# Kernel optimization log

Hardware: AMD Instinct MI355X
Metric: run time of the kernel (lower is better)

Reference implementation:

```python
import jax, jax.numpy as jnp
import numpy as np

B, T, TOKEN_DIM, TPR_DIM = 16, 256, 256, 10
INNER = TOKEN_DIM // 4  # 64
TH = 32                 # tpr_mlp hidden dim
EPS = 1e-5              # BatchNorm eps


def _bn(x, g, b, m, v):
    # BatchNorm1d in eval mode: normalize with running stats
    return (x - m) * jax.lax.rsqrt(v + EPS) * g + b


def setup_inputs() -> dict:
    key = jax.random.key(0)
    ks = iter(jax.random.split(key, 32))
    def n(shape, s=0.02):
        return jax.random.normal(next(ks), shape, dtype=jnp.float32) * s
    def bn_params(c):
        g = 1.0 + 0.1 * jax.random.normal(next(ks), (c,), dtype=jnp.float32)
        b = 0.1 * jax.random.normal(next(ks), (c,), dtype=jnp.float32)
        m = 0.1 * jax.random.normal(next(ks), (c,), dtype=jnp.float32)
        v = jax.random.uniform(next(ks), (c,), dtype=jnp.float32, minval=0.5, maxval=1.5)
        return g, b, m, v
    inp = {}
    inp['x'] = jax.random.normal(next(ks), (B, T, TOKEN_DIM), dtype=jnp.float32)
    inp['r'] = jax.random.normal(next(ks), (B, T, T, TPR_DIM), dtype=jnp.float32)
    # fc1: Linear(token,token) + BN(token)
    inp['W1'] = n((TOKEN_DIM, TOKEN_DIM)); inp['b1'] = n((TOKEN_DIM,))
    inp['bn1_g'], inp['bn1_b'], inp['bn1_m'], inp['bn1_v'] = bn_params(TOKEN_DIM)
    # VectorAttention
    inp['Wqkv'] = n((TOKEN_DIM, 3 * INNER))
    inp['Wt1'] = n((TPR_DIM, TH)); inp['bt1'] = n((TH,))
    inp['bnt_g'], inp['bnt_b'], inp['bnt_m'], inp['bnt_v'] = bn_params(TH)
    inp['Wt2'] = n((TH, INNER)); inp['bt2'] = n((INNER,))
    inp['Wa1'] = n((INNER, INNER)); inp['ba1'] = n((INNER,))
    inp['Wa2'] = n((INNER, INNER)); inp['ba2'] = n((INNER,))
    # fc2: Linear(inner, token) + BN(token)
    inp['W2'] = n((INNER, TOKEN_DIM)); inp['b2'] = n((TOKEN_DIM,))
    inp['bn2_g'], inp['bn2_b'], inp['bn2_m'], inp['bn2_v'] = bn_params(TOKEN_DIM)
    return inp


def reference(x, r, W1, b1, bn1_g, bn1_b, bn1_m, bn1_v, Wqkv,
              Wt1, bt1, bnt_g, bnt_b, bnt_m, bnt_v, Wt2, bt2,
              Wa1, ba1, Wa2, ba2, W2, b2, bn2_g, bn2_b, bn2_m, bn2_v):
    # fc1 + BN, residual skip (pre-relu)
    y = _bn(x @ W1 + b1, bn1_g, bn1_b, bn1_m, bn1_v)  # [B,T,C]
    skip = y
    y = jax.nn.relu(y)
    # VectorAttention
    qkv = y @ Wqkv                                     # [B,T,3*inner]
    q, k, v = jnp.split(qkv, 3, axis=-1)               # each [B,T,inner]
    qk_rel = q[:, :, None, :] - k[:, None, :, :]       # [B,T,T,inner]
    rel_emb = jax.nn.relu(_bn(r @ Wt1 + bt1, bnt_g, bnt_b, bnt_m, bnt_v)) @ Wt2 + bt2  # [B,T,T,inner]
    vv = v[:, None, :, :] + rel_emb                    # [B,T,T,inner]
    h = jax.nn.relu((qk_rel + rel_emb) @ Wa1 + ba1)
    sim = h @ Wa2 + ba2                                # [B,T,T,inner]
    attn = jax.nn.softmax(sim, axis=-2)                # softmax over j (neighbor) axis
    agg = jnp.sum(attn * vv, axis=2)                   # [B,T,inner]
    # fc2 + BN + residual + relu
    out = jax.nn.relu(_bn(agg @ W2 + b2, bn2_g, bn2_b, bn2_m, bn2_v) + skip)
    return out  # [B,T,token_dim]
```

## Files before the change

### kernel.cpp

```cpp
#include <hip/hip_runtime.h>
#include <hip/hip_bf16.h>
#include <math.h>

#define BB 16
#define TT 256
#define CC 256
#define INNER 64
#define TPR 10
#define THD 32
#define EPSV 1e-5f

typedef __attribute__((ext_vector_type(8))) short short8;
typedef __attribute__((ext_vector_type(4))) float f32x4;

__device__ __forceinline__ short f2bf(float f) {
    unsigned u = __float_as_uint(f);
    u += 0x7fffu + ((u >> 16) & 1);
    return (short)(u >> 16);
}
__device__ __forceinline__ unsigned cvtpk(float a, float b) {
    __hip_bfloat162 h = __float22bfloat162_rn(float2{a, b});
    return *(unsigned*)&h;
}

#define IMG_WT1  0
#define IMG_WT2  2048
#define IMG_WA1  6144
#define IMG_WA2  14336
#define IMG_C1   22528
#define IMG_SZ   22656

__device__ __forceinline__ int sww(int pb, int key) {
    return ((pb & ~15) ^ key) | (pb & 15);
}

__global__ __launch_bounds__(256) void prep_kernel(
    const float* __restrict__ Wt1, const float* __restrict__ bt1,
    const float* __restrict__ gt, const float* __restrict__ bbt,
    const float* __restrict__ mt, const float* __restrict__ vt,
    const float* __restrict__ Wt2, const float* __restrict__ Wa1,
    const float* __restrict__ Wa2, char* __restrict__ img)
{
    const int blk = blockIdx.x, t = threadIdx.x;
    if (blk == 0) {
        for (int e = t; e < 32 * 32; e += 256) {
            int m = e >> 5, k = e & 31;
            float scv = gt[m] * rsqrtf(vt[m] + EPSV);
            float v = (k < TPR) ? Wt1[k * 32 + m] * scv : 0.f;
            *(short*)(img + IMG_WT1 + m * 64 + k * 2) = f2bf(v);
        }
        if (t < 32) {
            float scv = gt[t] * rsqrtf(vt[t] + EPSV);
            ((float*)(img + IMG_C1))[t] = (bt1[t] - mt[t]) * scv + bbt[t];
        }
    } else if (blk == 1) {
        for (int e = t; e < 32 * 64; e += 256) {
            int h = e >> 6, c = e & 63;
            int off = IMG_WT2 + (c >> 1) * 128 + sww((c & 1) * 64 + h * 2, ((c >> 1) & 7) << 4);
            *(short*)(img + off) = f2bf(Wt2[e]);
        }
    } else {
        const float* W = (blk == 2) ? Wa1 : Wa2;
        int base = (blk == 2) ? IMG_WA1 : IMG_WA2;
        for (int e = t; e < 64 * 64; e += 256) {
            int k = e >> 6, c = e & 63;
            int off = base + c * 128 + sww(k * 2, (c & 7) << 4);
            *(short*)(img + off) = f2bf(W[e]);
        }
    }
}

__global__ __launch_bounds__(256) void fc1_qkv_kernel(
    const float* __restrict__ x, const float* __restrict__ W1, const float* __restrict__ b1,
    const float* __restrict__ g1, const float* __restrict__ bb1,
    const float* __restrict__ m1, const float* __restrict__ v1,
    const float* __restrict__ Wqkv,
    float* __restrict__ skip, float* __restrict__ qkv)
{
    const int ROWS = 8;
    __shared__ float xr[ROWS][CC];
    __shared__ float yr[ROWS][CC];
    const int n0 = blockIdx.x * ROWS;
    const int t = threadIdx.x;

#pragma unroll
    for (int rr = 0; rr < ROWS; ++rr)
        xr[rr][t] = x[(size_t)(n0 + rr) * CC + t];
    __syncthreads();

    float acc[ROWS];
#pragma unroll
    for (int rr = 0; rr < ROWS; ++rr) acc[rr] = 0.f;
    for (int k = 0; k < CC; ++k) {
        float wv = W1[(size_t)k * CC + t];
#pragma unroll
        for (int rr = 0; rr < ROWS; ++rr) acc[rr] = fmaf(xr[rr][k], wv, acc[rr]);
    }
    const float s1 = g1[t] * rsqrtf(v1[t] + EPSV);
    const float base = b1[t] - m1[t];
    const float bet = bb1[t];
#pragma unroll
    for (int rr = 0; rr < ROWS; ++rr) {
        float y = (acc[rr] + base) * s1 + bet;
        skip[(size_t)(n0 + rr) * CC + t] = y;
        yr[rr][t] = fmaxf(y, 0.f);
    }
    __syncthreads();

    if (t < 192) {
        float a2[ROWS];
#pragma unroll
        for (int rr = 0; rr < ROWS; ++rr) a2[rr] = 0.f;
        for (int k = 0; k < CC; ++k) {
            float wv = Wqkv[(size_t)k * 192 + t];
#pragma unroll
            for (int rr = 0; rr < ROWS; ++rr) a2[rr] = fmaf(yr[rr][k], wv, a2[rr]);
        }
#pragma unroll
        for (int rr = 0; rr < ROWS; ++rr)
            qkv[(size_t)(n0 + rr) * 192 + t] = a2[rr];
    }
}

#define O_R    0
#define O_TH   16384
#define O_WT1  49152
#define O_WT2  51200
#define O_WA1  55296
#define O_WA2  63488
#define O_RED  71680
#define LDSZ   75776

__device__ __forceinline__ int swb(int row, int cb, int sh, int mask) {
    return (row << sh) + (((cb & ~15) ^ ((row & mask) << 4)) | (cb & 15));
}
__device__ __forceinline__ short8 ldfrag(const char* lds, int base, int row, int cb16, int sh, int mask) {
    return *(const short8*)(lds + base + (row << sh) + (cb16 ^ ((row & mask) << 4)));
}

__global__ __launch_bounds__(512, 4) void attn_mfma_kernel(
    const float* __restrict__ r, const float* __restrict__ qkv,
    const float* __restrict__ bt2, const float* __restrict__ ba1,
    const char* __restrict__ img, float* __restrict__ agg)
{
    __shared__ __align__(16) char lds[LDSZ];
    const int n = blockIdx.x, b = n >> 8;
    const int tid = threadIdx.x;
    const int wv = tid >> 6, lane = tid & 63;
    const int lid = lane & 15, q4 = lane >> 4;
    const int kb = q4 * 16;
    const int jt0 = wv * 2;

    const float* kvb = qkv + (size_t)b * (TT * 192);
    const f32x4 z4 = {0.f, 0.f, 0.f, 0.f};

#pragma unroll
    for (int ci = 0; ci < 3; ++ci) {
        int c = wv + ci * 8;
        if (c < 22) {
            int ldsoff;
            if (c < 2)       ldsoff = O_WT1 + c * 1024;
            else if (c < 6)  ldsoff = O_WT2 + (c - 2) * 1024;
            else if (c < 14) ldsoff = O_WA1 + (c - 6) * 1024;
            else             ldsoff = O_WA2 + (c - 14) * 1024;
            __builtin_amdgcn_global_load_lds(
                (const __attribute__((address_space(1))) unsigned*)(const unsigned*)(img + c * 1024 + lane * 16),
                (__attribute__((address_space(3))) unsigned*)(unsigned*)(lds + ldsoff + lane * 16),
                16, 0, 0);
        }
    }

    f32x4 k4[4][2];
#pragma unroll
    for (int tm = 0; tm < 4; ++tm) {
        int ch0 = tm * 16 + q4 * 4;
#pragma unroll
        for (int tn = 0; tn < 2; ++tn) {
            int j = (jt0 + tn) * 16 + lid;
            k4[tm][tn] = *(const f32x4*)(kvb + (size_t)j * 192 + 64 + ch0);
        }
    }

    {
        const float* rrow = r + (size_t)n * (TT * TPR);
        int j = tid >> 1, half = tid & 1;
        const float* rp = rrow + j * TPR + half * 5;
        float v0 = rp[0], v1 = rp[1], v2 = rp[2], v3 = rp[3], v4 = rp[4];
        char* rb = lds + O_R + j * 64;
        if (half == 0) {
            uint2 w; w.x = cvtpk(v0, v1); w.y = cvtpk(v2, v3);
            *(uint2*)(rb) = w;
            *(unsigned short*)(rb + 8) = (unsigned short)f2bf(v4);
        } else {
            *(unsigned short*)(rb + 10) = (unsigned short)f2bf(v0);
            *(unsigned*)(rb + 12) = cvtpk(v1, v2);
            *(unsigned*)(rb + 16) = cvtpk(v3, v4);
            *(unsigned*)(rb + 20) = 0u;
            uint2 zz; zz.x = 0u; zz.y = 0u;
            *(uint2*)(rb + 24) = zz;
            *(uint2*)(rb + 32) = zz;
            *(uint2*)(rb + 40) = zz;
            *(uint2*)(rb + 48) = zz;
            *(uint2*)(rb + 56) = zz;
        }
    }
    __syncthreads();

    const float* c1g = (const float*)(img + IMG_C1);

    {
        short8 a10 = ldfrag(lds, O_WT1, lid, kb, 6, 0);
        short8 a11 = ldfrag(lds, O_WT1, 16 + lid, kb, 6, 0);
        f32x4 c1v0 = *(const f32x4*)(c1g + q4 * 4);
        f32x4 c1v1 = *(const f32x4*)(c1g + 16 + q4 * 4);
        f32x4 acc1[2][2];
#pragma unroll
        for (int tn = 0; tn < 2; ++tn) {
            int j = (jt0 + tn) * 16 + lid;
            short8 bf = ldfrag(lds, O_R, j, kb, 6, 0);
            acc1[0][tn] = __builtin_amdgcn_mfma_f32_16x16x32_bf16(a10, bf, c1v0, 0, 0, 0);
            acc1[1][tn] = __builtin_amdgcn_mfma_f32_16x16x32_bf16(a11, bf, c1v1, 0, 0, 0);
        }
#pragma unroll
        for (int tm = 0; tm < 2; ++tm)
#pragma unroll
            for (int tn = 0; tn < 2; ++tn) {
                int j = (jt0 + tn) * 16 + lid;
                uint2 w;
                w.x = cvtpk(fmaxf(acc1[tm][tn][0], 0.f), fmaxf(acc1[tm][tn][1], 0.f));
                w.y = cvtpk(fmaxf(acc1[tm][tn][2], 0.f), fmaxf(acc1[tm][tn][3], 0.f));
                *(uint2*)(lds + O_TH + swb(j, tm * 32 + q4 * 8, 7, 7)) = w;
            }
    }

    f32x4 qv4[4], bt2v[4];
#pragma unroll
    for (int tm = 0; tm < 4; ++tm) {
        int ch0 = tm * 16 + q4 * 4;
        qv4[tm] = *(const f32x4*)(qkv + (size_t)n * 192 + ch0);
        bt2v[tm] = *(const f32x4*)(bt2 + ch0);
    }

    f32x4 rel[4][2];
    {
        short8 aw[4];
#pragma unroll
        for (int tm = 0; tm < 4; ++tm) {
            int c = tm * 16 + lid;
            aw[tm] = ldfrag(lds, O_WT2, c >> 1, (c & 1) * 64 + kb, 7, 7);
        }
#pragma unroll
        for (int tn = 0; tn < 2; ++tn) {
            int j = (jt0 + tn) * 16 + lid;
            short8 bf = ldfrag(lds, O_TH, j, kb, 7, 7);
#pragma unroll
            for (int tm = 0; tm < 4; ++tm)
                rel[tm][tn] = __builtin_amdgcn_mfma_f32_16x16x32_bf16(aw[tm], bf, bt2v[tm], 0, 0, 0);
        }
    }
#pragma unroll
    for (int tm = 0; tm < 4; ++tm)
#pragma unroll
        for (int tn = 0; tn < 2; ++tn) {
            int j = (jt0 + tn) * 16 + lid;
            float t0 = qv4[tm][0] - k4[tm][tn][0] + rel[tm][tn][0];
            float t1 = qv4[tm][1] - k4[tm][tn][1] + rel[tm][tn][1];
            float t2 = qv4[tm][2] - k4[tm][tn][2] + rel[tm][tn][2];
            float t3 = qv4[tm][3] - k4[tm][tn][3] + rel[tm][tn][3];
            uint2 w; w.x = cvtpk(t0, t1); w.y = cvtpk(t2, t3);
            *(uint2*)(lds + O_TH + swb(j, tm * 32 + q4 * 8, 7, 7)) = w;
        }

    f32x4 ba1v[4];
#pragma unroll
    for (int tm = 0; tm < 4; ++tm)
        ba1v[tm] = *(const f32x4*)(ba1 + tm * 16 + q4 * 4);
    f32x4 acc[4][2];
#pragma unroll
    for (int tm = 0; tm < 4; ++tm)
#pragma unroll
        for (int tn = 0; tn < 2; ++tn) acc[tm][tn] = ba1v[tm];
#pragma unroll
    for (int ks = 0; ks < 2; ++ks) {
        short8 aw[4];
#pragma unroll
        for (int tm = 0; tm < 4; ++tm)
            aw[tm] = ldfrag(lds, O_WA1, tm * 16 + lid, ks * 64 + kb, 7, 7);
#pragma unroll
        for (int tn = 0; tn < 2; ++tn) {
            int j = (jt0 + tn) * 16 + lid;
            short8 bf = ldfrag(lds, O_TH, j, ks * 64 + kb, 7, 7);
#pragma unroll
            for (int tm = 0; tm < 4; ++tm)
                acc[tm][tn] = __builtin_amdgcn_mfma_f32_16x16x32_bf16(aw[tm], bf, acc[tm][tn], 0, 0, 0);
        }
    }

    f32x4 v4h[4][2];
#pragma unroll
    for (int tm = 0; tm < 4; ++tm) {
        int ch0 = tm * 16 + q4 * 4;
#pragma unroll
        for (int tn = 0; tn < 2; ++tn) {
            int j = (jt0 + tn) * 16 + lid;
            v4h[tm][tn] = *(const f32x4*)(kvb + (size_t)j * 192 + 128 + ch0);
        }
    }

#pragma unroll
    for (int tm = 0; tm < 4; ++tm)
#pragma unroll
        for (int tn = 0; tn < 2; ++tn) {
            int j = (jt0 + tn) * 16 + lid;
            uint2 w;
            w.x = cvtpk(fmaxf(acc[tm][tn][0], 0.f), fmaxf(acc[tm][tn][1], 0.f));
            w.y = cvtpk(fmaxf(acc[tm][tn][2], 0.f), fmaxf(acc[tm][tn][3], 0.f));
            *(uint2*)(lds + O_TH + swb(j, tm * 32 + q4 * 8, 7, 7)) = w;
        }

#pragma unroll
    for (int tm = 0; tm < 4; ++tm)
#pragma unroll
        for (int tn = 0; tn < 2; ++tn) acc[tm][tn] = z4;
#pragma unroll
    for (int ks = 0; ks < 2; ++ks) {
        short8 aw[4];
#pragma unroll
        for (int tm = 0; tm < 4; ++tm)
            aw[tm] = ldfrag(lds, O_WA2, tm * 16 + lid, ks * 64 + kb, 7, 7);
#pragma unroll
        for (int tn = 0; tn < 2; ++tn) {
            int j = (jt0 + tn) * 16 + lid;
            short8 bf = ldfrag(lds, O_TH, j, ks * 64 + kb, 7, 7);
#pragma unroll
            for (int tm = 0; tm < 4; ++tm)
                acc[tm][tn] = __builtin_amdgcn_mfma_f32_16x16x32_bf16(aw[tm], bf, acc[tm][tn], 0, 0, 0);
        }
    }

#pragma unroll
    for (int tm = 0; tm < 4; ++tm) {
        f32x4 num = z4, den = z4;
#pragma unroll
        for (int tn = 0; tn < 2; ++tn) {
#pragma unroll
            for (int g = 0; g < 4; ++g) {
                float ev = __expf(acc[tm][tn][g]);
                den[g] += ev;
                num[g] = fmaf(ev, v4h[tm][tn][g] + rel[tm][tn][g], num[g]);
            }
        }
#pragma unroll
        for (int ofs = 1; ofs < 16; ofs <<= 1) {
#pragma unroll
            for (int g = 0; g < 4; ++g) {
                num[g] += __shfl_xor(num[g], ofs);
                den[g] += __shfl_xor(den[g], ofs);
            }
        }
        if (lid == 0) {
            int base = O_RED + ((wv * 4 + tm) * 4 + q4) * 32;
            *(f32x4*)(lds + base) = num;
            *(f32x4*)(lds + base + 16) = den;
        }
    }
    __syncthreads();

    if (tid < 64) {
        int tm = tid >> 4, qq = (tid >> 2) & 3, g = tid & 3;
        float nn = 0.f, dd = 0.f;
#pragma unroll
        for (int w = 0; w < 8; ++w) {
            int base = O_RED + ((w * 4 + tm) * 4 + qq) * 32 + g * 4;
            nn += *(const float*)(lds + base);
            dd += *(const float*)(lds + base + 16);
        }
        agg[(size_t)n * 64 + tid] = nn / dd;
    }
}

__global__ __launch_bounds__(256) void fc2_kernel(
    const float* __restrict__ agg, const float* __restrict__ W2, const float* __restrict__ b2,
    const float* __restrict__ g2, const float* __restrict__ bb2,
    const float* __restrict__ m2, const float* __restrict__ v2,
    const float* __restrict__ skip, float* __restrict__ out)
{
    const int ROWS = 8;
    __shared__ float ar[ROWS][INNER];
    const int n0 = blockIdx.x * ROWS;
    const int t = threadIdx.x;

    for (int idx = t; idx < ROWS * INNER; idx += 256)
        ((float*)ar)[idx] = agg[(size_t)n0 * INNER + idx];
    __syncthreads();

    const float s2 = g2[t] * rsqrtf(v2[t] + EPSV);
    const float base = b2[t] - m2[t];
    const float bet = bb2[t];

    float accv[ROWS];
#pragma unroll
    for (int rr = 0; rr < ROWS; ++rr) accv[rr] = 0.f;
    for (int k = 0; k < INNER; ++k) {
        float wv = W2[(size_t)k * CC + t];
#pragma unroll
        for (int rr = 0; rr < ROWS; ++rr) accv[rr] = fmaf(ar[rr][k], wv, accv[rr]);
    }
#pragma unroll
    for (int rr = 0; rr < ROWS; ++rr) {
        float y = (accv[rr] + base) * s2 + bet;
        out[(size_t)(n0 + rr) * CC + t] =
            fmaxf(y + skip[(size_t)(n0 + rr) * CC + t], 0.f);
    }
}

extern "C" void kernel_launch(void* const* d_in, const int* in_sizes, int n_in,
                              void* d_out, int out_size, void* d_ws, size_t ws_size,
                              hipStream_t stream)
{
    const float* x   = (const float*)d_in[0];
    const float* r   = (const float*)d_in[1];
    const float* W1  = (const float*)d_in[2];
    const float* b1  = (const float*)d_in[3];
    const float* g1  = (const float*)d_in[4];
    const float* bb1 = (const float*)d_in[5];
    const float* m1  = (const float*)d_in[6];
    const float* v1  = (const float*)d_in[7];
    const float* Wqkv= (const float*)d_in[8];
    const float* Wt1 = (const float*)d_in[9];
    const float* bt1 = (const float*)d_in[10];
    const float* gt  = (const float*)d_in[11];
    const float* bbt = (const float*)d_in[12];
    const float* mt  = (const float*)d_in[13];
    const float* vt  = (const float*)d_in[14];
    const float* Wt2 = (const float*)d_in[15];
    const float* bt2 = (const float*)d_in[16];
    const float* Wa1 = (const float*)d_in[17];
    const float* ba1 = (const float*)d_in[18];
    const float* Wa2 = (const float*)d_in[19];
    const float* W2  = (const float*)d_in[21];
    const float* b2  = (const float*)d_in[22];
    const float* g2  = (const float*)d_in[23];
    const float* bb2 = (const float*)d_in[24];
    const float* m2  = (const float*)d_in[25];
    const float* v2  = (const float*)d_in[26];
    float* out = (float*)d_out;

    const int N = BB * TT;
    float* skip = (float*)d_ws;
    float* qkv  = skip + (size_t)N * CC;
    float* agg  = qkv  + (size_t)N * 192;
    char*  img  = (char*)(agg + (size_t)N * 64);

    prep_kernel<<<dim3(4), dim3(256), 0, stream>>>(
        Wt1, bt1, gt, bbt, mt, vt, Wt2, Wa1, Wa2, img);
    fc1_qkv_kernel<<<dim3(N / 8), dim3(256), 0, stream>>>(
        x, W1, b1, g1, bb1, m1, v1, Wqkv, skip, qkv);
    attn_mfma_kernel<<<dim3(N), dim3(512), 0, stream>>>(
        r, qkv, bt2, ba1, img, agg);
    fc2_kernel<<<dim3(N / 8), dim3(256), 0, stream>>>(
        agg, W2, b2, g2, bb2, m2, v2, skip, out);
}
```

Measured before the change: 160.5 us.

## Pack q-k and v+rel into bf16 registers, pad r rows, relax launch bounds

```diff
diff --git a/kernel.cpp b/kernel.cpp
--- a/kernel.cpp
+++ b/kernel.cpp
@@ -12,6 +12,7 @@
 
 typedef __attribute__((ext_vector_type(8))) short short8;
 typedef __attribute__((ext_vector_type(4))) float f32x4;
+typedef __attribute__((ext_vector_type(4))) unsigned int u32x4;
 
 __device__ __forceinline__ short f2bf(float f) {
     unsigned u = __float_as_uint(f);
@@ -22,6 +23,8 @@
     __hip_bfloat162 h = __float22bfloat162_rn(float2{a, b});
     return *(unsigned*)&h;
 }
+__device__ __forceinline__ float bf_lo(unsigned u) { return __uint_as_float(u << 16); }
+__device__ __forceinline__ float bf_hi(unsigned u) { return __uint_as_float(u & 0xffff0000u); }
 
 #define IMG_WT1  0
 #define IMG_WT2  2048
@@ -123,13 +126,13 @@
 }
 
 #define O_R    0
-#define O_TH   16384
-#define O_WT1  49152
-#define O_WT2  51200
-#define O_WA1  55296
-#define O_WA2  63488
-#define O_RED  71680
-#define LDSZ   75776
+#define O_TH   20480
+#define O_WT1  53248
+#define O_WT2  55296
+#define O_WA1  59392
+#define O_WA2  67584
+#define O_RED  75776
+#define LDSZ   79872
 
 __device__ __forceinline__ int swb(int row, int cb, int sh, int mask) {
     return (row << sh) + (((cb & ~15) ^ ((row & mask) << 4)) | (cb & 15));
@@ -138,7 +141,7 @@
     return *(const short8*)(lds + base + (row << sh) + (cb16 ^ ((row & mask) << 4)));
 }
 
-__global__ __launch_bounds__(512, 4) void attn_mfma_kernel(
+__global__ __launch_bounds__(512, 2) void attn_mfma_kernel(
     const float* __restrict__ r, const float* __restrict__ qkv,
     const float* __restrict__ bt2, const float* __restrict__ ba1,
     const char* __restrict__ img, float* __restrict__ agg)
@@ -170,10 +173,11 @@
         }
     }
 
-    f32x4 k4[4][2];
+    f32x4 qv4[4], k4[4][2];
 #pragma unroll
     for (int tm = 0; tm < 4; ++tm) {
         int ch0 = tm * 16 + q4 * 4;
+        qv4[tm] = *(const f32x4*)(qkv + (size_t)n * 192 + ch0);
 #pragma unroll
         for (int tn = 0; tn < 2; ++tn) {
             int j = (jt0 + tn) * 16 + lid;
@@ -183,25 +187,25 @@
 
     {
         const float* rrow = r + (size_t)n * (TT * TPR);
-        int j = tid >> 1, half = tid & 1;
-        const float* rp = rrow + j * TPR + half * 5;
+        int j = tid >> 1, hf = tid & 1;
+        const float* rp = rrow + j * TPR + hf * 5;
         float v0 = rp[0], v1 = rp[1], v2 = rp[2], v3 = rp[3], v4 = rp[4];
-        char* rb = lds + O_R + j * 64;
-        if (half == 0) {
-            uint2 w; w.x = cvtpk(v0, v1); w.y = cvtpk(v2, v3);
-            *(uint2*)(rb) = w;
-            *(unsigned short*)(rb + 8) = (unsigned short)f2bf(v4);
+        float o0 = __shfl_xor(v0, 1);
+        float o1 = __shfl_xor(v1, 1);
+        float o2 = __shfl_xor(v2, 1);
+        char* rb = lds + O_R + j * 80;
+        u32x4 z = {0u, 0u, 0u, 0u};
+        if (hf == 0) {
+            u32x4 c;
+            c[0] = cvtpk(v0, v1); c[1] = cvtpk(v2, v3);
+            c[2] = cvtpk(v4, o0); c[3] = cvtpk(o1, o2);
+            *(u32x4*)(rb) = c;
+            *(u32x4*)(rb + 32) = z;
         } else {
-            *(unsigned short*)(rb + 10) = (unsigned short)f2bf(v0);
-            *(unsigned*)(rb + 12) = cvtpk(v1, v2);
-            *(unsigned*)(rb + 16) = cvtpk(v3, v4);
-            *(unsigned*)(rb + 20) = 0u;
-            uint2 zz; zz.x = 0u; zz.y = 0u;
-            *(uint2*)(rb + 24) = zz;
-            *(uint2*)(rb + 32) = zz;
-            *(uint2*)(rb + 40) = zz;
-            *(uint2*)(rb + 48) = zz;
-            *(uint2*)(rb + 56) = zz;
+            u32x4 c;
+            c[0] = cvtpk(v3, v4); c[1] = 0u; c[2] = 0u; c[3] = 0u;
+            *(u32x4*)(rb + 16) = c;
+            *(u32x4*)(rb + 48) = z;
         }
     }
     __syncthreads();
@@ -209,15 +213,15 @@
     const float* c1g = (const float*)(img + IMG_C1);
 
     {
-        short8 a10 = ldfrag(lds, O_WT1, lid, kb, 6, 0);
-        short8 a11 = ldfrag(lds, O_WT1, 16 + lid, kb, 6, 0);
+        short8 a10 = *(const short8*)(lds + O_WT1 + lid * 64 + kb);
+        short8 a11 = *(const short8*)(lds + O_WT1 + (16 + lid) * 64 + kb);
         f32x4 c1v0 = *(const f32x4*)(c1g + q4 * 4);
         f32x4 c1v1 = *(const f32x4*)(c1g + 16 + q4 * 4);
         f32x4 acc1[2][2];
 #pragma unroll
         for (int tn = 0; tn < 2; ++tn) {
             int j = (jt0 + tn) * 16 + lid;
-            short8 bf = ldfrag(lds, O_R, j, kb, 6, 0);
+            short8 bf = *(const short8*)(lds + O_R + j * 80 + kb);
             acc1[0][tn] = __builtin_amdgcn_mfma_f32_16x16x32_bf16(a10, bf, c1v0, 0, 0, 0);
             acc1[1][tn] = __builtin_amdgcn_mfma_f32_16x16x32_bf16(a11, bf, c1v1, 0, 0, 0);
         }
@@ -233,12 +237,25 @@
             }
     }
 
-    f32x4 qv4[4], bt2v[4];
+    uint2 pk[4][2];
+#pragma unroll
+    for (int tm = 0; tm < 4; ++tm)
+#pragma unroll
+        for (int tn = 0; tn < 2; ++tn) {
+            pk[tm][tn].x = cvtpk(qv4[tm][0] - k4[tm][tn][0], qv4[tm][1] - k4[tm][tn][1]);
+            pk[tm][tn].y = cvtpk(qv4[tm][2] - k4[tm][tn][2], qv4[tm][3] - k4[tm][tn][3]);
+        }
+
+    f32x4 v4h[4][2], bt2v[4];
 #pragma unroll
     for (int tm = 0; tm < 4; ++tm) {
         int ch0 = tm * 16 + q4 * 4;
-        qv4[tm] = *(const f32x4*)(qkv + (size_t)n * 192 + ch0);
         bt2v[tm] = *(const f32x4*)(bt2 + ch0);
+#pragma unroll
+        for (int tn = 0; tn < 2; ++tn) {
+            int j = (jt0 + tn) * 16 + lid;
+            v4h[tm][tn] = *(const f32x4*)(kvb + (size_t)j * 192 + 128 + ch0);
+        }
     }
 
     f32x4 rel[4][2];
@@ -258,17 +275,23 @@
                 rel[tm][tn] = __builtin_amdgcn_mfma_f32_16x16x32_bf16(aw[tm], bf, bt2v[tm], 0, 0, 0);
         }
     }
-#pragma unroll
-    for (int tm = 0; tm < 4; ++tm)
-#pragma unroll
-        for (int tn = 0; tn < 2; ++tn) {
-            int j = (jt0 + tn) * 16 + lid;
-            float t0 = qv4[tm][0] - k4[tm][tn][0] + rel[tm][tn][0];
-            float t1 = qv4[tm][1] - k4[tm][tn][1] + rel[tm][tn][1];
-            float t2 = qv4[tm][2] - k4[tm][tn][2] + rel[tm][tn][2];
-            float t3 = qv4[tm][3] - k4[tm][tn][3] + rel[tm][tn][3];
+
+    uint2 vvp[4][2];
+#pragma unroll
+    for (int tm = 0; tm < 4; ++tm)
+#pragma unroll
+        for (int tn = 0; tn < 2; ++tn) {
+            int j = (jt0 + tn) * 16 + lid;
+            float r0 = rel[tm][tn][0], r1 = rel[tm][tn][1];
+            float r2 = rel[tm][tn][2], r3 = rel[tm][tn][3];
+            float t0 = bf_lo(pk[tm][tn].x) + r0;
+            float t1 = bf_hi(pk[tm][tn].x) + r1;
+            float t2 = bf_lo(pk[tm][tn].y) + r2;
+            float t3 = bf_hi(pk[tm][tn].y) + r3;
             uint2 w; w.x = cvtpk(t0, t1); w.y = cvtpk(t2, t3);
             *(uint2*)(lds + O_TH + swb(j, tm * 32 + q4 * 8, 7, 7)) = w;
+            vvp[tm][tn].x = cvtpk(v4h[tm][tn][0] + r0, v4h[tm][tn][1] + r1);
+            vvp[tm][tn].y = cvtpk(v4h[tm][tn][2] + r2, v4h[tm][tn][3] + r3);
         }
 
     f32x4 ba1v[4];
@@ -295,18 +318,6 @@
                 acc[tm][tn] = __builtin_amdgcn_mfma_f32_16x16x32_bf16(aw[tm], bf, acc[tm][tn], 0, 0, 0);
         }
     }
-
-    f32x4 v4h[4][2];
-#pragma unroll
-    for (int tm = 0; tm < 4; ++tm) {
-        int ch0 = tm * 16 + q4 * 4;
-#pragma unroll
-        for (int tn = 0; tn < 2; ++tn) {
-            int j = (jt0 + tn) * 16 + lid;
-            v4h[tm][tn] = *(const f32x4*)(kvb + (size_t)j * 192 + 128 + ch0);
-        }
-    }
-
 #pragma unroll
     for (int tm = 0; tm < 4; ++tm)
 #pragma unroll
@@ -343,12 +354,16 @@
         f32x4 num = z4, den = z4;
 #pragma unroll
         for (int tn = 0; tn < 2; ++tn) {
-#pragma unroll
-            for (int g = 0; g < 4; ++g) {
-                float ev = __expf(acc[tm][tn][g]);
-                den[g] += ev;
-                num[g] = fmaf(ev, v4h[tm][tn][g] + rel[tm][tn][g], num[g]);
-            }
+            float vf0 = bf_lo(vvp[tm][tn].x), vf1 = bf_hi(vvp[tm][tn].x);
+            float vf2 = bf_lo(vvp[tm][tn].y), vf3 = bf_hi(vvp[tm][tn].y);
+            float e0 = __expf(acc[tm][tn][0]);
+            float e1 = __expf(acc[tm][tn][1]);
+            float e2 = __expf(acc[tm][tn][2]);
+            float e3 = __expf(acc[tm][tn][3]);
+            den[0] += e0; num[0] = fmaf(e0, vf0, num[0]);
+            den[1] += e1; num[1] = fmaf(e1, vf1, num[1]);
+            den[2] += e2; num[2] = fmaf(e2, vf2, num[2]);
+            den[3] += e3; num[3] = fmaf(e3, vf3, num[3]);
         }
 #pragma unroll
         for (int ofs = 1; ofs < 16; ofs <<= 1) {
```

Result: slower. 181.0 us (+12.8%).
